# Optimization experiments

Hardware: AMD Instinct MI355X
Metric: run time of the kernel (lower is better)

Reference implementation:

```python
import jax, jax.numpy as jnp
import numpy as np

N_NODES = 100000
N_EDGES = 640000
D_IN = 128
D_OUT = 128

def setup_inputs() -> dict:
    key = jax.random.key(0)
    k1, k2, k3, k4, k5 = jax.random.split(key, 5)
    feat = jax.random.normal(k1, (N_NODES, D_IN), dtype=jnp.float32)
    src = jax.random.randint(k2, (N_EDGES,), 0, N_NODES, dtype=jnp.int32)
    dst = jax.random.randint(k3, (N_EDGES,), 0, N_NODES, dtype=jnp.int32)
    scale = 1.0 / np.sqrt(D_IN)
    W_self = jax.random.normal(k4, (D_IN, D_OUT), dtype=jnp.float32) * scale
    W_neigh = jax.random.normal(k5, (D_IN, D_OUT), dtype=jnp.float32) * scale
    b_self = jnp.zeros((D_OUT,), dtype=jnp.float32)
    b_neigh = jnp.zeros((D_OUT,), dtype=jnp.float32)
    return {"feat": feat, "src": src, "dst": dst,
            "W_self": W_self, "b_self": b_self,
            "W_neigh": W_neigh, "b_neigh": b_neigh}

def reference(feat, src, dst, W_self, b_self, W_neigh, b_neigh):
    # GraphSAGE 'mean' aggregator: copy_src + mean reduce over in-edges, then
    # rst = fc_self(h_self) + fc_neigh(h_neigh). feat_drop=0, no activation/norm.
    n = feat.shape[0]
    msg = feat[src]                                   # [E, D_in] gather
    neigh_sum = jax.ops.segment_sum(msg, dst, num_segments=n)      # [N, D_in]
    deg = jax.ops.segment_sum(jnp.ones_like(dst, dtype=feat.dtype), dst,
                              num_segments=n)          # [N]
    # mean with zero-in-degree nodes -> 0 (DGL semantics)
    h_neigh = neigh_sum / jnp.maximum(deg, 1.0)[:, None]
    rst = feat @ W_self + b_self + h_neigh @ W_neigh + b_neigh      # [N, D_out]
    return rst
```

## Files before the change

kernel.cpp:

```cpp
#include <hip/hip_runtime.h>


constexpr int N_NODES = 100000;
constexpr int N_EDGES = 640000;
constexpr int D = 128;

constexpr int SCAN_ELEMS_PER_BLOCK = 1024;
constexpr int SCAN_NBLOCKS = (N_NODES + SCAN_ELEMS_PER_BLOCK - 1) / SCAN_ELEMS_PER_BLOCK;

typedef __attribute__((ext_vector_type(8))) short bf16x8;
typedef __attribute__((ext_vector_type(4))) float f32x4;
typedef __attribute__((ext_vector_type(2))) float f32x2;

__device__ __forceinline__ unsigned short f2bf(float f) {
    unsigned int u = __float_as_uint(f);
    unsigned int r = u + 0x7FFFu + ((u >> 16) & 1u);
    return (unsigned short)(r >> 16);
}


__global__ void deg_wprep_kernel(const int* __restrict__ dst, int* __restrict__ deg,
                                 const float* __restrict__ Ws, const float* __restrict__ Wn,
                                 unsigned short* __restrict__ wp) {
    int e = blockIdx.x * blockDim.x + threadIdx.x;
    if (e < N_EDGES) atomicAdd(&deg[dst[e]], 1);
    if (e < 2 * D * D) {
        int i = e;
        int r  = i & 7;
        int c  = (i >> 3) & 127;
        int h  = (i >> 10) & 3;
        int ks = (i >> 12) & 3;
        int m  = i >> 14;
        const float* W = m ? Wn : Ws;
        int k = ks * 32 + h * 8 + r;
        wp[i] = f2bf(W[k * D + c]);
    }
}

__global__ __launch_bounds__(256) void partial_kernel(const int* __restrict__ deg,
                                                      int* __restrict__ bsum) {
    __shared__ int wsum[4];
    const int tid = threadIdx.x;
    const int base = (blockIdx.x * 256 + tid) * 4;
    int s = 0;
    #pragma unroll
    for (int j = 0; j < 4; j++) {
        int idx = base + j;
        if (idx < N_NODES) s += deg[idx];
    }
    for (int off = 32; off > 0; off >>= 1) s += __shfl_down(s, off, 64);
    if ((tid & 63) == 0) wsum[tid >> 6] = s;
    __syncthreads();
    if (tid == 0) bsum[blockIdx.x] = wsum[0] + wsum[1] + wsum[2] + wsum[3];
}

__global__ __launch_bounds__(128) void scanb_kernel(const int* __restrict__ bsum,
                                                    int* __restrict__ boff,
                                                    int* __restrict__ rowptr) {
    __shared__ int s[128];
    const int tid = threadIdx.x;
    int v = (tid < SCAN_NBLOCKS) ? bsum[tid] : 0;
    s[tid] = v;
    __syncthreads();
    for (int off = 1; off < 128; off <<= 1) {
        int u = (tid >= off) ? s[tid - off] : 0;
        __syncthreads();
        s[tid] += u;
        __syncthreads();
    }
    if (tid < SCAN_NBLOCKS) boff[tid] = s[tid] - v;
    if (tid == 0) rowptr[N_NODES] = N_EDGES;
}

__global__ __launch_bounds__(256) void final_kernel(const int* __restrict__ deg,
                                                    const int* __restrict__ boff,
                                                    int* __restrict__ rowptr,
                                                    int* __restrict__ cursor) {
    __shared__ int wsum[4];
    const int tid = threadIdx.x;
    const int lane = tid & 63;
    const int wave = tid >> 6;
    const int base = (blockIdx.x * 256 + tid) * 4;

    int local[4];
    int tsum = 0;
    #pragma unroll
    for (int j = 0; j < 4; j++) {
        int idx = base + j;
        local[j] = (idx < N_NODES) ? deg[idx] : 0;
        tsum += local[j];
    }
    int incl = tsum;
    for (int off = 1; off < 64; off <<= 1) {
        int u = __shfl_up(incl, off, 64);
        if (lane >= off) incl += u;
    }
    if (lane == 63) wsum[wave] = incl;
    __syncthreads();
    int woff = 0;
    for (int w = 0; w < 4; w++) woff += (w < wave) ? wsum[w] : 0;

    int run = boff[blockIdx.x] + woff + (incl - tsum);
    #pragma unroll
    for (int j = 0; j < 4; j++) {
        int idx = base + j;
        if (idx < N_NODES) {
            rowptr[idx] = run;
            cursor[idx] = run;
            run += local[j];
        }
    }
}

__global__ void fill_kernel(const int* __restrict__ src, const int* __restrict__ dst,
                            int* __restrict__ cursor, int* __restrict__ csr_src) {
    int e = blockIdx.x * blockDim.x + threadIdx.x;
    if (e < N_EDGES) {
        int pos = atomicAdd(&cursor[dst[e]], 1);
        csr_src[pos] = src[e];
    }
}

__global__ __launch_bounds__(256) void mmfused_kernel(
    const float* __restrict__ feat, const unsigned short* __restrict__ wp,
    const float* __restrict__ b_self, const float* __restrict__ b_neigh,
    float* __restrict__ out, unsigned short* __restrict__ t)
{
    __shared__ unsigned short lw[2 * 4 * 4 * 128 * 8];

    const int tid = threadIdx.x;
    {
        const uint4* s = (const uint4*)wp;
        uint4* d = (uint4*)lw;
        #pragma unroll
        for (int i = 0; i < 16; i++) d[tid + i * 256] = s[tid + i * 256];
    }
    __syncthreads();

    const int wave = tid >> 6, lane = tid & 63;
    const int h = lane >> 4, c = lane & 15;
    const int row_base = blockIdx.x * 128 + wave * 32;

    bf16x8 a[2][4];
    #pragma unroll
    for (int ti = 0; ti < 2; ti++) {
        int row = row_base + ti * 16 + c;
        int rowc = min(row, N_NODES - 1);
        const float4* fr = (const float4*)(feat + (size_t)rowc * D);
        #pragma unroll
        for (int ks = 0; ks < 4; ks++) {
            float4 u = fr[ks * 8 + h * 2];
            float4 v = fr[ks * 8 + h * 2 + 1];
            bf16x8 f;
            f[0] = (short)f2bf(u.x); f[1] = (short)f2bf(u.y);
            f[2] = (short)f2bf(u.z); f[3] = (short)f2bf(u.w);
            f[4] = (short)f2bf(v.x); f[5] = (short)f2bf(v.y);
            f[6] = (short)f2bf(v.z); f[7] = (short)f2bf(v.w);
            a[ti][ks] = f;
        }
    }

    #pragma unroll
    for (int m = 0; m < 2; m++) {
        for (int ct = 0; ct < 8; ct++) {
            bf16x8 b[4];
            #pragma unroll
            for (int ks = 0; ks < 4; ks++)
                b[ks] = ((const bf16x8*)lw)[((m * 4 + ks) * 4 + h) * 128 + ct * 16 + c];

            f32x4 acc[2];
            #pragma unroll
            for (int ti = 0; ti < 2; ti++) acc[ti] = f32x4{0.f, 0.f, 0.f, 0.f};
            #pragma unroll
            for (int ks = 0; ks < 4; ks++)
                #pragma unroll
                for (int ti = 0; ti < 2; ti++)
                    acc[ti] = __builtin_amdgcn_mfma_f32_16x16x32_bf16(a[ti][ks], b[ks], acc[ti], 0, 0, 0);

            const int col = ct * 16 + c;
            if (m == 0) {
                const float bias = b_self[col] + b_neigh[col];
                #pragma unroll
                for (int ti = 0; ti < 2; ti++) {
                    if (row_base + ti * 16 < N_NODES) {
                        #pragma unroll
                        for (int q = 0; q < 4; q++) {
                            int row = row_base + ti * 16 + h * 4 + q;
                            out[(size_t)row * D + col] = acc[ti][q] + bias;
                        }
                    }
                }
            } else {
                #pragma unroll
                for (int ti = 0; ti < 2; ti++) {
                    if (row_base + ti * 16 < N_NODES) {
                        #pragma unroll
                        for (int q = 0; q < 4; q++) {
                            int row = row_base + ti * 16 + h * 4 + q;
                            t[(size_t)row * D + col] = f2bf(acc[ti][q]);
                        }
                    }
                }
            }
        }
    }
}

__global__ __launch_bounds__(256) void gather_kernel(
    const unsigned short* __restrict__ t, const int* __restrict__ csr_src,
    const int* __restrict__ rowptr, float* __restrict__ out)
{
    const int lane = threadIdx.x & 63;
    const int n = (blockIdx.x * blockDim.x + threadIdx.x) >> 6;
    if (n >= N_NODES) return;

    const int e0 = rowptr[n];
    const int e1 = rowptr[n + 1];

    f32x2* orow = (f32x2*)(out + (size_t)n * D) + lane;
    f32x2 o = __builtin_nontemporal_load(orow);

    float ax = 0.f, ay = 0.f;
    for (int base = e0; base < e1; base += 16) {
        const int cnt = min(16, e1 - base);
        int myidx = (lane < cnt) ? csr_src[base + lane] : 0;
        unsigned int vv[16];
        #pragma unroll
        for (int j = 0; j < 16; j++) {
            if (j < cnt) {
                int s = __builtin_amdgcn_readlane(myidx, j);
                vv[j] = ((const unsigned int*)(t + (size_t)s * D))[lane];
            }
        }
        #pragma unroll
        for (int j = 0; j < 16; j++) {
            if (j < cnt) {
                ax += __uint_as_float(vv[j] << 16);
                ay += __uint_as_float(vv[j] & 0xFFFF0000u);
            }
        }
    }
    const float sc = 1.0f / (float)max(e1 - e0, 1);
    o.x += ax * sc;
    o.y += ay * sc;
    __builtin_nontemporal_store(o, orow);
}

extern "C" void kernel_launch(void* const* d_in, const int* in_sizes, int n_in,
                              void* d_out, int out_size, void* d_ws, size_t ws_size,
                              hipStream_t stream) {
    const float* feat    = (const float*)d_in[0];
    const int*   src     = (const int*)d_in[1];
    const int*   dst     = (const int*)d_in[2];
    const float* W_self  = (const float*)d_in[3];
    const float* b_self  = (const float*)d_in[4];
    const float* W_neigh = (const float*)d_in[5];
    const float* b_neigh = (const float*)d_in[6];
    float* out = (float*)d_out;

    unsigned short* t  = (unsigned short*)d_ws;
    unsigned short* wp = t + (size_t)N_NODES * D;
    int*   deg     = (int*)(wp + 2 * D * D);
    int*   rowptr  = deg + N_NODES;
    int*   cursor  = rowptr + (N_NODES + 1);
    int*   csr_src = cursor + N_NODES;
    int*   bsum    = csr_src + N_EDGES;
    int*   boff    = bsum + SCAN_NBLOCKS;

    (void)hipMemsetAsync(deg, 0, N_NODES * sizeof(int), stream);
    deg_wprep_kernel<<<(N_EDGES + 255) / 256, 256, 0, stream>>>(dst, deg, W_self, W_neigh, wp);

    partial_kernel<<<SCAN_NBLOCKS, 256, 0, stream>>>(deg, bsum);
    scanb_kernel<<<1, 128, 0, stream>>>(bsum, boff, rowptr);
    final_kernel<<<SCAN_NBLOCKS, 256, 0, stream>>>(deg, boff, rowptr, cursor);

    fill_kernel<<<(N_EDGES + 255) / 256, 256, 0, stream>>>(src, dst, cursor, csr_src);

    mmfused_kernel<<<(N_NODES + 127) / 128, 256, 0, stream>>>(feat, wp, b_self, b_neigh, out, t);

    gather_kernel<<<25000, 256, 0, stream>>>(t, csr_src, rowptr, out);
}
```

Measured before the change: 160.2 us.

## Fuse CSR scan and fill into one persistent kernel with grid barriers

Result: no change. 158.0 us (-1.3%).

```diff
diff --git a/kernel.cpp b/kernel.cpp
--- a/kernel.cpp
+++ b/kernel.cpp
@@ -5,8 +5,8 @@
 constexpr int N_EDGES = 640000;
 constexpr int D = 128;
 
-constexpr int SCAN_ELEMS_PER_BLOCK = 1024;
-constexpr int SCAN_NBLOCKS = (N_NODES + SCAN_ELEMS_PER_BLOCK - 1) / SCAN_ELEMS_PER_BLOCK;
+constexpr int CSR_NBLOCKS = 98;
+constexpr int CSR_THREADS = 256;
 
 typedef __attribute__((ext_vector_type(8))) short bf16x8;
 typedef __attribute__((ext_vector_type(4))) float f32x4;
@@ -17,7 +17,6 @@
     unsigned int r = u + 0x7FFFu + ((u >> 16) & 1u);
     return (unsigned short)(r >> 16);
 }
-
 
 __global__ void deg_wprep_kernel(const int* __restrict__ dst, int* __restrict__ deg,
                                  const float* __restrict__ Ws, const float* __restrict__ Wn,
@@ -37,50 +36,28 @@
     }
 }
 
-__global__ __launch_bounds__(256) void partial_kernel(const int* __restrict__ deg,
-                                                      int* __restrict__ bsum) {
-    __shared__ int wsum[4];
-    const int tid = threadIdx.x;
-    const int base = (blockIdx.x * 256 + tid) * 4;
-    int s = 0;
-    #pragma unroll
-    for (int j = 0; j < 4; j++) {
-        int idx = base + j;
-        if (idx < N_NODES) s += deg[idx];
-    }
-    for (int off = 32; off > 0; off >>= 1) s += __shfl_down(s, off, 64);
-    if ((tid & 63) == 0) wsum[tid >> 6] = s;
-    __syncthreads();
-    if (tid == 0) bsum[blockIdx.x] = wsum[0] + wsum[1] + wsum[2] + wsum[3];
-}
-
-__global__ __launch_bounds__(128) void scanb_kernel(const int* __restrict__ bsum,
-                                                    int* __restrict__ boff,
-                                                    int* __restrict__ rowptr) {
-    __shared__ int s[128];
-    const int tid = threadIdx.x;
-    int v = (tid < SCAN_NBLOCKS) ? bsum[tid] : 0;
-    s[tid] = v;
-    __syncthreads();
-    for (int off = 1; off < 128; off <<= 1) {
-        int u = (tid >= off) ? s[tid - off] : 0;
-        __syncthreads();
-        s[tid] += u;
-        __syncthreads();
-    }
-    if (tid < SCAN_NBLOCKS) boff[tid] = s[tid] - v;
-    if (tid == 0) rowptr[N_NODES] = N_EDGES;
-}
-
-__global__ __launch_bounds__(256) void final_kernel(const int* __restrict__ deg,
-                                                    const int* __restrict__ boff,
-                                                    int* __restrict__ rowptr,
-                                                    int* __restrict__ cursor) {
+__device__ __forceinline__ void grid_barrier(int* ctr) {
+    __syncthreads();
+    if (threadIdx.x == 0) {
+        __threadfence();
+        __hip_atomic_fetch_add(ctr, 1, __ATOMIC_ACQ_REL, __HIP_MEMORY_SCOPE_AGENT);
+        while (__hip_atomic_load(ctr, __ATOMIC_ACQUIRE, __HIP_MEMORY_SCOPE_AGENT)
+               < CSR_NBLOCKS) {}
+    }
+    __syncthreads();
+}
+
+__global__ __launch_bounds__(CSR_THREADS) void csr_kernel(
+    const int* __restrict__ deg, const int* __restrict__ src,
+    const int* __restrict__ dst, int* __restrict__ rowptr,
+    int* __restrict__ cursor, int* __restrict__ csr_src,
+    int* __restrict__ bsum, int* __restrict__ ctr)
+{
     __shared__ int wsum[4];
     const int tid = threadIdx.x;
     const int lane = tid & 63;
     const int wave = tid >> 6;
-    const int base = (blockIdx.x * 256 + tid) * 4;
+    const int base = (blockIdx.x * CSR_THREADS + tid) * 4;
 
     int local[4];
     int tsum = 0;
@@ -90,17 +67,35 @@
         local[j] = (idx < N_NODES) ? deg[idx] : 0;
         tsum += local[j];
     }
+    {
+        int s = tsum;
+        for (int off = 32; off > 0; off >>= 1) s += __shfl_down(s, off, 64);
+        if (lane == 0) wsum[wave] = s;
+        __syncthreads();
+        if (tid == 0) bsum[blockIdx.x] = wsum[0] + wsum[1] + wsum[2] + wsum[3];
+    }
+
+    grid_barrier(&ctr[0]);
+
+    int v = (tid < blockIdx.x) ? bsum[tid] : 0;
+    for (int off = 32; off > 0; off >>= 1) v += __shfl_down(v, off, 64);
+    __syncthreads();
+    if (lane == 0) wsum[wave] = v;
+    __syncthreads();
+    const int boff = wsum[0] + wsum[1] + wsum[2] + wsum[3];
+
     int incl = tsum;
     for (int off = 1; off < 64; off <<= 1) {
         int u = __shfl_up(incl, off, 64);
         if (lane >= off) incl += u;
     }
+    __syncthreads();
     if (lane == 63) wsum[wave] = incl;
     __syncthreads();
     int woff = 0;
     for (int w = 0; w < 4; w++) woff += (w < wave) ? wsum[w] : 0;
 
-    int run = boff[blockIdx.x] + woff + (incl - tsum);
+    int run = boff + woff + (incl - tsum);
     #pragma unroll
     for (int j = 0; j < 4; j++) {
         int idx = base + j;
@@ -110,12 +105,12 @@
             run += local[j];
         }
     }
-}
-
-__global__ void fill_kernel(const int* __restrict__ src, const int* __restrict__ dst,
-                            int* __restrict__ cursor, int* __restrict__ csr_src) {
-    int e = blockIdx.x * blockDim.x + threadIdx.x;
-    if (e < N_EDGES) {
+    if (blockIdx.x == 0 && tid == 0) rowptr[N_NODES] = N_EDGES;
+
+    grid_barrier(&ctr[1]);
+
+    for (int e = blockIdx.x * CSR_THREADS + tid; e < N_EDGES;
+         e += CSR_NBLOCKS * CSR_THREADS) {
         int pos = atomicAdd(&cursor[dst[e]], 1);
         csr_src[pos] = src[e];
     }
@@ -221,23 +216,23 @@
     f32x2 o = __builtin_nontemporal_load(orow);
 
     float ax = 0.f, ay = 0.f;
-    for (int base = e0; base < e1; base += 16) {
-        const int cnt = min(16, e1 - base);
-        int myidx = (lane < cnt) ? csr_src[base + lane] : 0;
-        unsigned int vv[16];
-        #pragma unroll
-        for (int j = 0; j < 16; j++) {
-            if (j < cnt) {
-                int s = __builtin_amdgcn_readlane(myidx, j);
-                vv[j] = ((const unsigned int*)(t + (size_t)s * D))[lane];
-            }
-        }
-        #pragma unroll
-        for (int j = 0; j < 16; j++) {
-            if (j < cnt) {
-                ax += __uint_as_float(vv[j] << 16);
-                ay += __uint_as_float(vv[j] & 0xFFFF0000u);
-            }
+    for (int base = e0; base < e1; base += 8) {
+        int sidx[8];
+        #pragma unroll
+        for (int j = 0; j < 8; j++) {
+            int ee = base + j;
+            ee = (ee < e1) ? ee : (e1 - 1);
+            sidx[j] = csr_src[ee];
+        }
+        unsigned int v[8];
+        #pragma unroll
+        for (int j = 0; j < 8; j++)
+            v[j] = ((const unsigned int*)(t + (size_t)sidx[j] * D))[lane];
+        #pragma unroll
+        for (int j = 0; j < 8; j++) {
+            const float w = (base + j < e1) ? 1.0f : 0.0f;
+            ax = fmaf(w, __uint_as_float(v[j] << 16), ax);
+            ay = fmaf(w, __uint_as_float(v[j] & 0xFFFF0000u), ay);
         }
     }
     const float sc = 1.0f / (float)max(e1 - e0, 1);
@@ -265,16 +260,15 @@
     int*   cursor  = rowptr + (N_NODES + 1);
     int*   csr_src = cursor + N_NODES;
     int*   bsum    = csr_src + N_EDGES;
-    int*   boff    = bsum + SCAN_NBLOCKS;
+    int*   ctr     = bsum + CSR_NBLOCKS;
 
     (void)hipMemsetAsync(deg, 0, N_NODES * sizeof(int), stream);
+    (void)hipMemsetAsync(ctr, 0, 2 * sizeof(int), stream);
+
     deg_wprep_kernel<<<(N_EDGES + 255) / 256, 256, 0, stream>>>(dst, deg, W_self, W_neigh, wp);
 
-    partial_kernel<<<SCAN_NBLOCKS, 256, 0, stream>>>(deg, bsum);
-    scanb_kernel<<<1, 128, 0, stream>>>(bsum, boff, rowptr);
-    final_kernel<<<SCAN_NBLOCKS, 256, 0, stream>>>(deg, boff, rowptr, cursor);
-
-    fill_kernel<<<(N_EDGES + 255) / 256, 256, 0, stream>>>(src, dst, cursor, csr_src);
+    csr_kernel<<<CSR_NBLOCKS, CSR_THREADS, 0, stream>>>(deg, src, dst, rowptr,
+                                                        cursor, csr_src, bsum, ctr);
 
     mmfused_kernel<<<(N_NODES + 127) / 128, 256, 0, stream>>>(feat, wp, b_self, b_neigh, out, t);
 
```
